# Optimization experiments

Hardware: AMD Instinct MI355X
Metric: run time of the kernel (lower is better)

Reference implementation:

```python
import jax, jax.numpy as jnp
import numpy as np

DIM_EMB = 1024
NUM_HEADS = 16
DIM_HEAD = DIM_EMB // NUM_HEADS  # 64


def setup_inputs() -> dict:
    key = jax.random.key(0)
    k1, k2, k3 = jax.random.split(key, 3)
    x = jax.random.normal(k1, (4, 2048, DIM_EMB), dtype=jnp.float32)
    # nn.Linear(dim_embedding, 3*h*d, bias=False): weight shape [out, in]
    w_qkv = jax.random.normal(k2, (3 * NUM_HEADS * DIM_HEAD, DIM_EMB), dtype=jnp.float32) * (DIM_EMB ** -0.5)
    w_out = jax.random.normal(k3, (DIM_EMB, NUM_HEADS * DIM_HEAD), dtype=jnp.float32) * ((NUM_HEADS * DIM_HEAD) ** -0.5)
    return {"x": x, "w_qkv": w_qkv, "w_out": w_out}


def reference(x, w_qkv, w_out):
    b, t, _ = x.shape
    scale = DIM_HEAD ** -0.5
    qkv = jnp.einsum('bte,fe->btf', x, w_qkv)  # [b, t, 3*h*d]
    qkv = qkv.reshape(b, t, 3, NUM_HEADS, DIM_HEAD)  # fused dim order (k h d)
    q, k, v = qkv[:, :, 0], qkv[:, :, 1], qkv[:, :, 2]  # each [b, t, h, d]
    scores = jnp.einsum('bihd,bjhd->bhij', q, k) * scale  # [b, h, t, t]
    weights = jax.nn.softmax(scores, axis=-1)
    attn = jnp.einsum('bhij,bjhd->bhid', weights, v)  # [b, h, t, d]
    concat = attn.transpose(0, 2, 1, 3).reshape(b, t, NUM_HEADS * DIM_HEAD)
    return jnp.einsum('btf,ef->bte', concat, w_out)
```

## Files before the change

kernel.cpp:

```cpp
#include <hip/hip_runtime.h>

#define DI __device__ __forceinline__

typedef float  f32x4  __attribute__((ext_vector_type(4)));
typedef float  f32x16 __attribute__((ext_vector_type(16)));
typedef __bf16 bf16x8 __attribute__((ext_vector_type(8)));
typedef unsigned u32x2 __attribute__((ext_vector_type(2)));
typedef unsigned u32x4 __attribute__((ext_vector_type(4)));

static constexpr int TB   = 2048;
static constexpr int NTOK = 8192;
static constexpr int EMB  = 1024;
static constexpr int FQKV = 3072;

DI unsigned short f2bf(float f) {
  union { float f; unsigned u; } v; v.f = f;
  unsigned r = v.u + 0x7FFFu + ((v.u >> 16) & 1u);
  return (unsigned short)(r >> 16);
}

DI unsigned pack2bf(float a, float b) {
  unsigned ua = __builtin_bit_cast(unsigned, a) + 0x8000u;
  unsigned ub = __builtin_bit_cast(unsigned, b) + 0x8000u;
  return __builtin_amdgcn_perm(ub, ua, 0x07060302u);
}

DI void plswap(unsigned& a, unsigned& b) {
#if __has_builtin(__builtin_amdgcn_permlane32_swap)
  u32x2 r = __builtin_amdgcn_permlane32_swap(a, b, false, false);
  a = r.x; b = r.y;
#else
  const bool hi = (threadIdx.x & 32) != 0;
  unsigned ax = (unsigned)__shfl_xor((int)a, 32);
  unsigned bx = (unsigned)__shfl_xor((int)b, 32);
  unsigned na = hi ? bx : a;
  unsigned nb = hi ? b : ax;
  a = na; b = nb;
#endif
}

DI bf16x8 frag4(unsigned a, unsigned b, unsigned c, unsigned d) {
  u32x4 u = {a, b, c, d};
  return __builtin_bit_cast(bf16x8, u);
}

DI void gload16(const void* g, void* l) {
  __builtin_amdgcn_global_load_lds(
      (__attribute__((address_space(1))) void*)(g),
      (__attribute__((address_space(3))) void*)(l), 16, 0, 0);
}

__global__ __launch_bounds__(256)
void cvt_kernel(const float4* __restrict__ x, const float4* __restrict__ wq,
                const float4* __restrict__ wo,
                ushort4* __restrict__ xb, ushort4* __restrict__ wqb,
                ushort4* __restrict__ wob) {
  const int i  = blockIdx.x * 256 + threadIdx.x;
  const int nx = NTOK * EMB / 4;
  const int nq = FQKV * EMB / 4;
  float4 v; ushort4* dst;
  if (i < nx)           { v = x[i];           dst = xb  + i; }
  else if (i < nx + nq) { v = wq[i - nx];     dst = wqb + (i - nx); }
  else                  { v = wo[i - nx - nq]; dst = wob + (i - nx - nq); }
  ushort4 p;
  p.x = f2bf(v.x); p.y = f2bf(v.y); p.z = f2bf(v.z); p.w = f2bf(v.w);
  *dst = p;
}

template <int MODE>
__global__ __launch_bounds__(256)
void gemm_bt(const unsigned short* __restrict__ A,
             const unsigned short* __restrict__ Bt,
             const int K,
             unsigned short* __restrict__ qk,
             unsigned short* __restrict__ vT,
             float* __restrict__ outp) {
  __shared__ unsigned short sA[128 * 32];
  __shared__ unsigned short sB[128 * 32];
  const int tid  = threadIdx.x;
  const int w    = tid >> 6;
  const int l    = tid & 63;
  const int quad = l >> 4;
  const int lr   = l & 15;
  const int n0   = blockIdx.x * 128;
  const int m0   = blockIdx.y * 128;
  const int wm   = (w >> 1) * 64;
  const int wn   = (w & 1) * 64;

  f32x4 acc[4][4];
#pragma unroll
  for (int i = 0; i < 4; ++i)
#pragma unroll
    for (int j = 0; j < 4; ++j) acc[i][j] = {0.f, 0.f, 0.f, 0.f};

  const int srow = l >> 2;
  const int sg   = (l & 3) ^ ((l >> 3) & 3);
  const unsigned short* gA = A  + (long)(m0 + w * 32 + srow) * K + sg * 8;
  const unsigned short* gB = Bt + (long)(n0 + w * 32 + srow) * K + sg * 8;
  unsigned short* lA = sA + w * 1024;
  unsigned short* lB = sB + w * 1024;
  const int swz = (lr >> 1) & 3;

  for (int k0 = 0; k0 < K; k0 += 32) {
    gload16(gA + k0,          lA);
    gload16(gA + k0 + 16 * K, lA + 512);
    gload16(gB + k0,          lB);
    gload16(gB + k0 + 16 * K, lB + 512);
    __syncthreads();
    bf16x8 af[4], bfr[4];
#pragma unroll
    for (int rt = 0; rt < 4; ++rt)
      af[rt] = *(const bf16x8*)(sA + (wm + rt * 16 + lr) * 32 + (quad ^ swz) * 8);
#pragma unroll
    for (int ct = 0; ct < 4; ++ct)
      bfr[ct] = *(const bf16x8*)(sB + (wn + ct * 16 + lr) * 32 + (quad ^ swz) * 8);
#pragma unroll
    for (int rt = 0; rt < 4; ++rt)
#pragma unroll
      for (int ct = 0; ct < 4; ++ct)
        acc[rt][ct] = __builtin_amdgcn_mfma_f32_16x16x32_bf16(af[rt], bfr[ct],
                                                              acc[rt][ct], 0, 0, 0);
    __syncthreads();
  }

  if (MODE == 0) {
    if (n0 < 2048) {
      const float qs = (n0 < 1024) ? 0.18033688011112042f : 1.0f;
#pragma unroll
      for (int rt = 0; rt < 4; ++rt) {
        const int row = m0 + wm + rt * 16 + quad * 4;
#pragma unroll
        for (int ct = 0; ct < 4; ++ct) {
          const int col = n0 + wn + ct * 16 + lr;
#pragma unroll
          for (int r = 0; r < 4; ++r)
            qk[(long)(row + r) * 2048 + col] = f2bf(acc[rt][ct][r] * qs);
        }
      }
    } else {
#pragma unroll
      for (int rt = 0; rt < 4; ++rt) {
        const int tok = m0 + wm + rt * 16 + quad * 4;
        const int bb  = tok >> 11, tt = tok & 2047;
#pragma unroll
        for (int ct = 0; ct < 4; ++ct) {
          const int fv = n0 - 2048 + wn + ct * 16 + lr;
          ushort4 p;
          p.x = f2bf(acc[rt][ct][0]); p.y = f2bf(acc[rt][ct][1]);
          p.z = f2bf(acc[rt][ct][2]); p.w = f2bf(acc[rt][ct][3]);
          *(ushort4*)(vT + ((long)(bb * 1024 + fv)) * 2048 + tt) = p;
        }
      }
    }
  } else {
#pragma unroll
    for (int rt = 0; rt < 4; ++rt) {
      const int row = m0 + wm + rt * 16 + quad * 4;
#pragma unroll
      for (int ct = 0; ct < 4; ++ct) {
        const int col = n0 + wn + ct * 16 + lr;
#pragma unroll
        for (int r = 0; r < 4; ++r)
          outp[(long)(row + r) * 1024 + col] = acc[rt][ct][r];
      }
    }
  }
}

__global__ __launch_bounds__(256)
void attn_kernel(const unsigned short* __restrict__ qk,
                 const unsigned short* __restrict__ vT,
                 unsigned short* __restrict__ attnb) {
  __shared__ unsigned short sK[2][64 * 64];
  __shared__ unsigned short sV[2][64 * 64];
  const int tid = threadIdx.x;
  const int w   = tid >> 6;
  const int l   = tid & 63;
  const int l31 = l & 31;
  const int lh  = l >> 5;
  const int h8  = lh * 8;
  const int bh  = blockIdx.y;
  const int hh  = bh & 15;
  const long tokbase = (long)(bh >> 4) * TB;
  const int q0  = blockIdx.x * 128 + w * 32;

  const unsigned short* qptr = qk + (tokbase + q0 + l31) * 2048 + hh * 64 + h8;
  bf16x8 qf[4];
#pragma unroll
  for (int s = 0; s < 4; ++s) qf[s] = *(const bf16x8*)(qptr + s * 16);

  const int srow = l >> 3;
  const int g    = (l & 7) ^ srow;
  const unsigned short* kbase =
      qk + (tokbase + w * 16 + srow) * 2048 + 1024 + hh * 64 + g * 8;
  const unsigned short* vbase =
      vT + ((long)bh * 64 + w * 16 + srow) * 2048 + g * 8;

  f32x16 oacc0 = {}, oacc1 = {};
  float lp = 0.f;

  gload16(kbase,                 &sK[0][(w * 16 + 0) * 64]);
  gload16(kbase + 8 * 2048,      &sK[0][(w * 16 + 8) * 64]);
  gload16(vbase,                 &sV[0][(w * 16 + 0) * 64]);
  gload16(vbase + 8 * 2048,      &sV[0][(w * 16 + 8) * 64]);
  __syncthreads();

  for (int t = 0; t < 32; ++t) {
    const int buf = t & 1;
    if (t + 1 < 32) {
      const int k0 = (t + 1) * 64;
      const int nb = buf ^ 1;
      gload16(kbase + (long)k0 * 2048,            &sK[nb][(w * 16 + 0) * 64]);
      gload16(kbase + (long)k0 * 2048 + 8 * 2048, &sK[nb][(w * 16 + 8) * 64]);
      gload16(vbase + k0,                         &sV[nb][(w * 16 + 0) * 64]);
      gload16(vbase + k0 + 8 * 2048,              &sV[nb][(w * 16 + 8) * 64]);
    }
    const unsigned short* bK = sK[buf];
    const unsigned short* bV = sV[buf];

#pragma unroll
    for (int G = 0; G < 2; ++G) {
      f32x16 sacc = {};
#pragma unroll
      for (int s = 0; s < 4; ++s) {
        const int key = G * 32 + l31;
        const int p   = (s * 2 + lh) ^ (key & 7);
        const bf16x8 kf = *(const bf16x8*)(bK + key * 64 + p * 8);
        sacc = __builtin_amdgcn_mfma_f32_32x32x16_bf16(kf, qf[s], sacc, 0, 0, 0);
      }
      float e[16];
#pragma unroll
      for (int i = 0; i < 16; ++i) {
        e[i] = __builtin_amdgcn_exp2f(sacc[i]);
        lp += e[i];
      }
      unsigned d[8];
#pragma unroll
      for (int i = 0; i < 8; ++i) d[i] = pack2bf(e[2 * i], e[2 * i + 1]);
      plswap(d[0], d[2]); plswap(d[1], d[3]);
      plswap(d[4], d[6]); plswap(d[5], d[7]);
      const bf16x8 p0 = frag4(d[0], d[1], d[2], d[3]);
      const bf16x8 p1 = frag4(d[4], d[5], d[6], d[7]);

#pragma unroll
      for (int sub = 0; sub < 2; ++sub) {
        const int kg = G * 2 + sub;
        const bf16x8 pp = sub ? p1 : p0;
        const int gt  = kg * 2 + lh;
        const int d0r = l31, d1r = 32 + l31;
        const bf16x8 vf0 = *(const bf16x8*)(bV + d0r * 64 + ((gt ^ (d0r & 7))) * 8);
        const bf16x8 vf1 = *(const bf16x8*)(bV + d1r * 64 + ((gt ^ (d1r & 7))) * 8);
        oacc0 = __builtin_amdgcn_mfma_f32_32x32x16_bf16(pp, vf0, oacc0, 0, 0, 0);
        oacc1 = __builtin_amdgcn_mfma_f32_32x32x16_bf16(pp, vf1, oacc1, 0, 0, 0);
      }
    }
    __syncthreads();
  }

  const float fs = lp + __shfl_xor(lp, 32);
  const float rc = 1.0f / fs;
#pragma unroll
  for (int r = 0; r < 16; ++r) {
    const int row = (r & 3) + 8 * (r >> 2) + 4 * lh;
    const float sc = __shfl(rc, row);
    const long base = (tokbase + q0 + row) * 1024 + hh * 64;
    attnb[base + l31]      = f2bf(oacc0[r] * sc);
    attnb[base + 32 + l31] = f2bf(oacc1[r] * sc);
  }
}

extern "C" void kernel_launch(void* const* d_in, const int* in_sizes, int n_in,
                              void* d_out, int out_size, void* d_ws, size_t ws_size,
                              hipStream_t stream) {
  const float* x    = (const float*)d_in[0];
  const float* wqkv = (const float*)d_in[1];
  const float* wout = (const float*)d_in[2];
  float* outp = (float*)d_out;

  unsigned short* xb    = (unsigned short*)d_ws;
  unsigned short* wqkvb = xb    + (long)NTOK * EMB;
  unsigned short* woutb = wqkvb + (long)FQKV * EMB;
  unsigned short* qkb   = woutb + (long)EMB * EMB;
  unsigned short* vTb   = qkb   + (long)NTOK * 2048;
  unsigned short* attnb = vTb   + (long)4 * 16 * 64 * TB;

  cvt_kernel<<<12288, 256, 0, stream>>>(
      (const float4*)x, (const float4*)wqkv, (const float4*)wout,
      (ushort4*)xb, (ushort4*)wqkvb, (ushort4*)woutb);

  gemm_bt<0><<<dim3(24, 64), 256, 0, stream>>>(xb, wqkvb, EMB, qkb, vTb, nullptr);

  attn_kernel<<<dim3(16, 64), 256, 0, stream>>>(qkb, vTb, attnb);

  gemm_bt<1><<<dim3(8, 64), 256, 0, stream>>>(attnb, woutb, EMB, nullptr, nullptr, outp);
}
```

Before: 296.9 us.

## Process 64 queries per wave in attention to reuse K/V fragments

The attention kernel now gives each wave two 32-query sub-tiles (256 queries per block), so every K and V fragment read from LDS feeds twice as many MFMAs. The grid is reordered so blockIdx.x indexes batch-head and block count drops to 512. The change also adds a packed bf16 convert builtin for the probability packing, vectorised row-sum accumulation, and an explicit waitcnt(0) before each barrier in both kernels. The cost is higher register pressure from double the accumulators and fewer blocks for occupancy.

```diff
diff --git a/kernel.cpp b/kernel.cpp
--- a/kernel.cpp
+++ b/kernel.cpp
@@ -2,6 +2,7 @@
 
 #define DI __device__ __forceinline__
 
+typedef float  f32x2  __attribute__((ext_vector_type(2)));
 typedef float  f32x4  __attribute__((ext_vector_type(4)));
 typedef float  f32x16 __attribute__((ext_vector_type(16)));
 typedef __bf16 bf16x8 __attribute__((ext_vector_type(8)));
@@ -20,9 +21,15 @@
 }
 
 DI unsigned pack2bf(float a, float b) {
+#if __has_builtin(__builtin_amdgcn_cvt_pk_bf16_f32)
+  typedef __bf16 bf16x2 __attribute__((ext_vector_type(2)));
+  bf16x2 r = __builtin_amdgcn_cvt_pk_bf16_f32(a, b);
+  return __builtin_bit_cast(unsigned, r);
+#else
   unsigned ua = __builtin_bit_cast(unsigned, a) + 0x8000u;
   unsigned ub = __builtin_bit_cast(unsigned, b) + 0x8000u;
   return __builtin_amdgcn_perm(ub, ua, 0x07060302u);
+#endif
 }
 
 DI void plswap(unsigned& a, unsigned& b) {
@@ -48,6 +55,11 @@
   __builtin_amdgcn_global_load_lds(
       (__attribute__((address_space(1))) void*)(g),
       (__attribute__((address_space(3))) void*)(l), 16, 0, 0);
+}
+
+DI void syncdrain() {
+  __builtin_amdgcn_s_waitcnt(0);
+  __syncthreads();
 }
 
 __global__ __launch_bounds__(256)
@@ -106,7 +118,7 @@
     gload16(gA + k0 + 16 * K, lA + 512);
     gload16(gB + k0,          lB);
     gload16(gB + k0 + 16 * K, lB + 512);
-    __syncthreads();
+    syncdrain();
     bf16x8 af[4], bfr[4];
 #pragma unroll
     for (int rt = 0; rt < 4; ++rt)
@@ -179,15 +191,19 @@
   const int l31 = l & 31;
   const int lh  = l >> 5;
   const int h8  = lh * 8;
-  const int bh  = blockIdx.y;
+  const int bh  = blockIdx.x;
   const int hh  = bh & 15;
   const long tokbase = (long)(bh >> 4) * TB;
-  const int q0  = blockIdx.x * 128 + w * 32;
-
-  const unsigned short* qptr = qk + (tokbase + q0 + l31) * 2048 + hh * 64 + h8;
-  bf16x8 qf[4];
-#pragma unroll
-  for (int s = 0; s < 4; ++s) qf[s] = *(const bf16x8*)(qptr + s * 16);
+  const int qbase = blockIdx.y * 256 + w * 64;
+
+  bf16x8 qf[2][4];
+#pragma unroll
+  for (int qs = 0; qs < 2; ++qs) {
+    const unsigned short* qptr =
+        qk + (tokbase + qbase + qs * 32 + l31) * 2048 + hh * 64 + h8;
+#pragma unroll
+    for (int s = 0; s < 4; ++s) qf[qs][s] = *(const bf16x8*)(qptr + s * 16);
+  }
 
   const int srow = l >> 3;
   const int g    = (l & 7) ^ srow;
@@ -196,14 +212,14 @@
   const unsigned short* vbase =
       vT + ((long)bh * 64 + w * 16 + srow) * 2048 + g * 8;
 
-  f32x16 oacc0 = {}, oacc1 = {};
-  float lp = 0.f;
-
-  gload16(kbase,                 &sK[0][(w * 16 + 0) * 64]);
-  gload16(kbase + 8 * 2048,      &sK[0][(w * 16 + 8) * 64]);
-  gload16(vbase,                 &sV[0][(w * 16 + 0) * 64]);
-  gload16(vbase + 8 * 2048,      &sV[0][(w * 16 + 8) * 64]);
-  __syncthreads();
+  f32x16 oacc[2][2] = {{{}, {}}, {{}, {}}};
+  f32x2 lp2[2] = {{0.f, 0.f}, {0.f, 0.f}};
+
+  gload16(kbase,            &sK[0][(w * 16 + 0) * 64]);
+  gload16(kbase + 8 * 2048, &sK[0][(w * 16 + 8) * 64]);
+  gload16(vbase,            &sV[0][(w * 16 + 0) * 64]);
+  gload16(vbase + 8 * 2048, &sV[0][(w * 16 + 8) * 64]);
+  syncdrain();
 
   for (int t = 0; t < 32; ++t) {
     const int buf = t & 1;
@@ -220,52 +236,63 @@
 
 #pragma unroll
     for (int G = 0; G < 2; ++G) {
-      f32x16 sacc = {};
+      f32x16 sacc[2] = {{}, {}};
 #pragma unroll
       for (int s = 0; s < 4; ++s) {
         const int key = G * 32 + l31;
         const int p   = (s * 2 + lh) ^ (key & 7);
         const bf16x8 kf = *(const bf16x8*)(bK + key * 64 + p * 8);
-        sacc = __builtin_amdgcn_mfma_f32_32x32x16_bf16(kf, qf[s], sacc, 0, 0, 0);
-      }
-      float e[16];
-#pragma unroll
-      for (int i = 0; i < 16; ++i) {
-        e[i] = __builtin_amdgcn_exp2f(sacc[i]);
-        lp += e[i];
-      }
-      unsigned d[8];
-#pragma unroll
-      for (int i = 0; i < 8; ++i) d[i] = pack2bf(e[2 * i], e[2 * i + 1]);
-      plswap(d[0], d[2]); plswap(d[1], d[3]);
-      plswap(d[4], d[6]); plswap(d[5], d[7]);
-      const bf16x8 p0 = frag4(d[0], d[1], d[2], d[3]);
-      const bf16x8 p1 = frag4(d[4], d[5], d[6], d[7]);
-
+        sacc[0] = __builtin_amdgcn_mfma_f32_32x32x16_bf16(kf, qf[0][s], sacc[0], 0, 0, 0);
+        sacc[1] = __builtin_amdgcn_mfma_f32_32x32x16_bf16(kf, qf[1][s], sacc[1], 0, 0, 0);
+      }
+      bf16x8 pp[2][2];
+#pragma unroll
+      for (int qs = 0; qs < 2; ++qs) {
+        float e[16];
+#pragma unroll
+        for (int i = 0; i < 16; ++i) e[i] = __builtin_amdgcn_exp2f(sacc[qs][i]);
+#pragma unroll
+        for (int i = 0; i < 8; ++i) {
+          f32x2 pr = {e[2 * i], e[2 * i + 1]};
+          lp2[qs] += pr;
+        }
+        unsigned d[8];
+#pragma unroll
+        for (int i = 0; i < 8; ++i) d[i] = pack2bf(e[2 * i], e[2 * i + 1]);
+        plswap(d[0], d[2]); plswap(d[1], d[3]);
+        plswap(d[4], d[6]); plswap(d[5], d[7]);
+        pp[qs][0] = frag4(d[0], d[1], d[2], d[3]);
+        pp[qs][1] = frag4(d[4], d[5], d[6], d[7]);
+      }
 #pragma unroll
       for (int sub = 0; sub < 2; ++sub) {
-        const int kg = G * 2 + sub;
-        const bf16x8 pp = sub ? p1 : p0;
-        const int gt  = kg * 2 + lh;
+        const int gt  = (G * 2 + sub) * 2 + lh;
         const int d0r = l31, d1r = 32 + l31;
         const bf16x8 vf0 = *(const bf16x8*)(bV + d0r * 64 + ((gt ^ (d0r & 7))) * 8);
         const bf16x8 vf1 = *(const bf16x8*)(bV + d1r * 64 + ((gt ^ (d1r & 7))) * 8);
-        oacc0 = __builtin_amdgcn_mfma_f32_32x32x16_bf16(pp, vf0, oacc0, 0, 0, 0);
-        oacc1 = __builtin_amdgcn_mfma_f32_32x32x16_bf16(pp, vf1, oacc1, 0, 0, 0);
-      }
-    }
-    __syncthreads();
-  }
-
-  const float fs = lp + __shfl_xor(lp, 32);
-  const float rc = 1.0f / fs;
-#pragma unroll
-  for (int r = 0; r < 16; ++r) {
-    const int row = (r & 3) + 8 * (r >> 2) + 4 * lh;
-    const float sc = __shfl(rc, row);
-    const long base = (tokbase + q0 + row) * 1024 + hh * 64;
-    attnb[base + l31]      = f2bf(oacc0[r] * sc);
-    attnb[base + 32 + l31] = f2bf(oacc1[r] * sc);
+#pragma unroll
+        for (int qs = 0; qs < 2; ++qs) {
+          oacc[qs][0] = __builtin_amdgcn_mfma_f32_32x32x16_bf16(pp[qs][sub], vf0, oacc[qs][0], 0, 0, 0);
+          oacc[qs][1] = __builtin_amdgcn_mfma_f32_32x32x16_bf16(pp[qs][sub], vf1, oacc[qs][1], 0, 0, 0);
+        }
+      }
+    }
+    syncdrain();
+  }
+
+#pragma unroll
+  for (int qs = 0; qs < 2; ++qs) {
+    const float lp = lp2[qs].x + lp2[qs].y;
+    const float fs = lp + __shfl_xor(lp, 32);
+    const float rc = 1.0f / fs;
+#pragma unroll
+    for (int r = 0; r < 16; ++r) {
+      const int row = (r & 3) + 8 * (r >> 2) + 4 * lh;
+      const float sc = __shfl(rc, row);
+      const long base = (tokbase + qbase + qs * 32 + row) * 1024 + hh * 64;
+      attnb[base + l31]      = f2bf(oacc[qs][0][r] * sc);
+      attnb[base + 32 + l31] = f2bf(oacc[qs][1][r] * sc);
+    }
   }
 }
 
@@ -290,7 +317,7 @@
 
   gemm_bt<0><<<dim3(24, 64), 256, 0, stream>>>(xb, wqkvb, EMB, qkb, vTb, nullptr);
 
-  attn_kernel<<<dim3(16, 64), 256, 0, stream>>>(qkb, vTb, attnb);
+  attn_kernel<<<dim3(64, 8), 256, 0, stream>>>(qkb, vTb, attnb);
 
   gemm_bt<1><<<dim3(8, 64), 256, 0, stream>>>(attnb, woutb, EMB, nullptr, nullptr, outp);
 }
```

Measured after the change: 275.9 us. -7.1%, faster.
